# Optimization experiments

Hardware: AMD Instinct MI355X
Metric: run time of the kernel (lower is better)

The kernel has to match this reference:

```python
import jax, jax.numpy as jnp
import numpy as np

B, T, I, H = 64, 512, 256, 256


def setup_inputs() -> dict:
    key = jax.random.key(0)
    ks = jax.random.split(key, 5)
    s = 1.0 / np.sqrt(H)
    return {
        "x": jax.random.normal(ks[0], (B, T, I), dtype=jnp.float32),
        "W_ih": jax.random.uniform(ks[1], (4 * H, I), jnp.float32, -s, s),
        "W_hh": jax.random.uniform(ks[2], (4 * H, H), jnp.float32, -s, s),
        "b_ih": jax.random.uniform(ks[3], (4 * H,), jnp.float32, -s, s),
        "b_hh": jax.random.uniform(ks[4], (4 * H,), jnp.float32, -s, s),
    }


def reference(x, W_ih, W_hh, b_ih, b_hh):
    # PyTorch LSTM gate order: input, forget, cell(g), output.
    # Precompute input projection for all timesteps: [B, T, 4H]
    x_proj = jnp.einsum("bti,gi->btg", x, W_ih) + b_ih + b_hh

    def step(carry, xt):
        h, c = carry                       # [B, H] each
        gates = xt + h @ W_hh.T            # [B, 4H]
        i, f, g, o = jnp.split(gates, 4, axis=-1)
        i = jax.nn.sigmoid(i)
        f = jax.nn.sigmoid(f)
        g = jnp.tanh(g)
        o = jax.nn.sigmoid(o)
        c = f * c + i * g
        h = o * jnp.tanh(c)
        return (h, c), h

    h0 = jnp.zeros((x.shape[0], W_hh.shape[1]), x.dtype)
    c0 = jnp.zeros_like(h0)
    (hT, cT), ys = jax.lax.scan(step, (h0, c0), jnp.swapaxes(x_proj, 0, 1))
    y = jnp.swapaxes(ys, 0, 1)             # [B, T, H], batch_first
    # Matches torch: (output, (h_n, c_n)) with num_layers*num_dirs = 1
    return y, hT[None], cT[None]
```

## Files before the change

kernel.cpp:

```cpp
#include <hip/hip_runtime.h>
#include <hip/hip_bf16.h>
#include <stdint.h>

#define Bz 64
#define Tz 512
#define Iz 256
#define Hz 256
#define G4z 1024
#define YSZ (Bz*Tz*Hz)

typedef __bf16 bf16;
typedef float  f32x4  __attribute__((ext_vector_type(4)));
typedef int    i32x4  __attribute__((ext_vector_type(4)));
typedef __bf16 bf16x8 __attribute__((ext_vector_type(8)));
typedef __bf16 bf16x4 __attribute__((ext_vector_type(4)));

#define XP_OFF  0u
#define XB_OFF  67108864u
#define WI_OFF  83886080u

__global__ __launch_bounds__(256) void cvt_f32_bf16(const float* __restrict__ in,
                                                    bf16* __restrict__ out, int n4) {
  int i = blockIdx.x * blockDim.x + threadIdx.x;
  if (i >= n4) return;
  float4 v = reinterpret_cast<const float4*>(in)[i];
  bf16x4 o = {(__bf16)v.x, (__bf16)v.y, (__bf16)v.z, (__bf16)v.w};
  *reinterpret_cast<bf16x4*>(out + (size_t)i*4) = o;
}

__global__ __launch_bounds__(256) void xproj_gemm(const bf16* __restrict__ A,
                                                  const bf16* __restrict__ Bw,
                                                  const float* __restrict__ b_ih,
                                                  const float* __restrict__ b_hh,
                                                  bf16* __restrict__ xp) {
  constexpr int K = 256;
  __shared__ __align__(16) bf16 As[128*32];
  __shared__ __align__(16) bf16 Bs[128*32];
  __shared__ float bias_s[128];
  const int bm = blockIdx.x >> 3;
  const int bn = blockIdx.x & 7;
  const int m0 = bm * 128, n0 = bn * 128;
  const int tid = threadIdx.x;
  if (tid < 128) bias_s[tid] = b_ih[n0 + tid] + b_hh[n0 + tid];
  const int w = tid >> 6, lane = tid & 63;
  const int wm = w >> 1, wn = w & 1;
  const int lr = lane & 15, lk = lane >> 4;
  f32x4 acc[4][4] = {};
  for (int kt = 0; kt < 8; ++kt) {
#pragma unroll
    for (int p = 0; p < 2; ++p) {
      int elem = p * 256 + tid;
      int row = elem >> 2, c = elem & 3;
      uint4 va = *reinterpret_cast<const uint4*>(A + (size_t)(m0 + row) * K + kt*32 + c*8);
      *reinterpret_cast<uint4*>((char*)As + row*64 + ((c ^ (row & 3)) * 16)) = va;
      uint4 vb = *reinterpret_cast<const uint4*>(Bw + (size_t)(n0 + row) * K + kt*32 + c*8);
      *reinterpret_cast<uint4*>((char*)Bs + row*64 + ((c ^ (row & 3)) * 16)) = vb;
    }
    __syncthreads();
    bf16x8 fa[4], fb[4];
#pragma unroll
    for (int f = 0; f < 4; ++f) {
      int ra = wm*64 + f*16 + lr;
      fa[f] = *reinterpret_cast<const bf16x8*>((char*)As + ra*64 + ((lk ^ (ra & 3)) * 16));
      int rb = wn*64 + f*16 + lr;
      fb[f] = *reinterpret_cast<const bf16x8*>((char*)Bs + rb*64 + ((lk ^ (rb & 3)) * 16));
    }
#pragma unroll
    for (int fi = 0; fi < 4; ++fi)
#pragma unroll
      for (int fj = 0; fj < 4; ++fj)
        acc[fi][fj] = __builtin_amdgcn_mfma_f32_16x16x32_bf16(fa[fi], fb[fj], acc[fi][fj], 0, 0, 0);
    __syncthreads();
  }
#pragma unroll
  for (int fi = 0; fi < 4; ++fi)
#pragma unroll
    for (int fj = 0; fj < 4; ++fj) {
      int col = n0 + wn*64 + fj*16 + lr;
      float bias = bias_s[wn*64 + fj*16 + lr];
#pragma unroll
      for (int v = 0; v < 4; ++v) {
        int row = m0 + wm*64 + fi*16 + lk*4 + v;
        xp[(size_t)row * 1024 + col] = (__bf16)(acc[fi][fj][v] + bias);
      }
    }
}


__device__ __forceinline__ float fast_sigmoid(float x) {
  return __builtin_amdgcn_rcpf(1.f + __expf(-x));
}
__device__ __forceinline__ float fast_tanh(float x) {
  return 1.f - 2.f * __builtin_amdgcn_rcpf(__expf(2.f * x) + 1.f);
}
__device__ __forceinline__ int sdot4f(int a, int b, int c) {
#if __has_builtin(__builtin_amdgcn_sdot4)
  return __builtin_amdgcn_sdot4(a, b, c, false);
#else
  int r = c;
  r += (int)(signed char)(a)        * (int)(signed char)(b);
  r += (int)(signed char)(a >> 8)   * (int)(signed char)(b >> 8);
  r += (int)(signed char)(a >> 16)  * (int)(signed char)(b >> 16);
  r += (int)(signed char)(a >> 24)  * (int)(signed char)(b >> 24);
  return r;
#endif
}
#define SCL (1.0f / (2032.0f * 127.0f))

__global__ __launch_bounds__(512, 2) void lstm_rec(const bf16* __restrict__ xp,
                                                   const float* __restrict__ Whh,
                                                   float* __restrict__ out) {
  __shared__ __align__(16) char  h_s[256];
  __shared__ float gates[1024];
  const int tid = threadIdx.x;
  const int b = blockIdx.x;

  int w0[64], w1[64];
  {
    const float* wp0 = Whh + (size_t)tid * 256;
    const float* wp1 = Whh + (size_t)(tid + 512) * 256;
#pragma unroll
    for (int d = 0; d < 64; ++d) {
      float4 f = *reinterpret_cast<const float4*>(wp0 + d*4);
      int q0 = (int)rintf(f.x * 2032.f), q1 = (int)rintf(f.y * 2032.f);
      int q2 = (int)rintf(f.z * 2032.f), q3 = (int)rintf(f.w * 2032.f);
      w0[d] = (q0 & 255) | ((q1 & 255) << 8) | ((q2 & 255) << 16) | ((q3 & 255) << 24);
      float4 g = *reinterpret_cast<const float4*>(wp1 + d*4);
      int p0 = (int)rintf(g.x * 2032.f), p1 = (int)rintf(g.y * 2032.f);
      int p2 = (int)rintf(g.z * 2032.f), p3 = (int)rintf(g.w * 2032.f);
      w1[d] = (p0 & 255) | ((p1 & 255) << 8) | ((p2 & 255) << 16) | ((p3 & 255) << 24);
    }
  }
  if (tid < 64) reinterpret_cast<int*>(h_s)[tid] = 0;

  const bf16* xprow = xp + (size_t)b * Tz * 1024;
  unsigned short x0v = *(const unsigned short*)(xprow + tid);
  unsigned short x1v = *(const unsigned short*)(xprow + 512 + tid);

  float cc = 0.f;
  __syncthreads();

  for (int t = 0; t < Tz; ++t) {
    int a0=0,a1=0,a2=0,a3=0, d0=0,d1=0,d2=0,d3=0;
#pragma unroll
    for (int d = 0; d < 16; ++d) {
      i32x4 hv = *reinterpret_cast<const i32x4*>(h_s + d*16);
      a0 = sdot4f(hv[0], w0[4*d+0], a0);
      a1 = sdot4f(hv[1], w0[4*d+1], a1);
      a2 = sdot4f(hv[2], w0[4*d+2], a2);
      a3 = sdot4f(hv[3], w0[4*d+3], a3);
      d0 = sdot4f(hv[0], w1[4*d+0], d0);
      d1 = sdot4f(hv[1], w1[4*d+1], d1);
      d2 = sdot4f(hv[2], w1[4*d+2], d2);
      d3 = sdot4f(hv[3], w1[4*d+3], d3);
    }
    float x0f = __uint_as_float((unsigned)x0v << 16);
    float x1f = __uint_as_float((unsigned)x1v << 16);
    gates[tid]       = (float)((a0 + a1) + (a2 + a3)) * SCL + x0f;
    gates[tid + 512] = (float)((d0 + d1) + (d2 + d3)) * SCL + x1f;
    if (t < Tz - 1) {
      x0v = *(const unsigned short*)(xprow + (size_t)(t+1)*1024 + tid);
      x1v = *(const unsigned short*)(xprow + (size_t)(t+1)*1024 + 512 + tid);
    }
    __syncthreads();

    if (tid < 256) {
      float gi = fast_sigmoid(gates[tid]);
      float gf = fast_sigmoid(gates[256 + tid]);
      float gg = fast_tanh(gates[512 + tid]);
      float go = fast_sigmoid(gates[768 + tid]);
      cc = gf * cc + gi * gg;
      float hv = go * fast_tanh(cc);
      out[((size_t)b * Tz + t) * 256 + tid] = hv;
      if (t < Tz - 1) {
        h_s[tid] = (char)(int)rintf(hv * 127.f);
      } else {
        out[(size_t)YSZ + (size_t)b * 256 + tid] = hv;
        out[(size_t)YSZ + 16384 + (size_t)b * 256 + tid] = cc;
      }
    }
    __syncthreads();
  }
}

extern "C" void kernel_launch(void* const* d_in, const int* in_sizes, int n_in,
                              void* d_out, int out_size, void* d_ws, size_t ws_size,
                              hipStream_t stream) {
  const float* x    = (const float*)d_in[0];
  const float* W_ih = (const float*)d_in[1];
  const float* W_hh = (const float*)d_in[2];
  const float* b_ih = (const float*)d_in[3];
  const float* b_hh = (const float*)d_in[4];
  float* out = (float*)d_out;
  char* ws = (char*)d_ws;

  bf16* xp  = (bf16*)(ws + XP_OFF);
  bf16* xb  = (bf16*)(ws + XB_OFF);
  bf16* wib = (bf16*)(ws + WI_OFF);

  cvt_f32_bf16<<<8192, 256, 0, stream>>>(x, xb, (Bz*Tz*Iz) / 4);
  cvt_f32_bf16<<<256, 256, 0, stream>>>(W_ih, wib, (G4z*Iz) / 4);
  xproj_gemm<<<2048, 256, 0, stream>>>(xb, wib, b_ih, b_hh, xp);
  lstm_rec<<<64, 512, 0, stream>>>(xp, W_hh, out);
}
```

Before: 573.4 us.

## Exchange LSTM gates via lane shuffles and double-buffer hidden state

Thread pairs now own all four gate rows for one hidden unit (i/f in one lane, g/o in the neighbor), so the gate values are exchanged with a lane xor shuffle instead of going through a shared-memory gates array. The hidden-state buffer is double-buffered, which removes one of the two block-wide barriers per timestep. Both lanes of each pair compute the cell update redundantly, and only the even lane writes outputs. This trades some duplicated transcendental work for shorter per-step serialization.

Result: slower. 604.3 us (+5.4%).

```diff
diff --git a/kernel.cpp b/kernel.cpp
--- a/kernel.cpp
+++ b/kernel.cpp
@@ -110,15 +110,18 @@
 __global__ __launch_bounds__(512, 2) void lstm_rec(const bf16* __restrict__ xp,
                                                    const float* __restrict__ Whh,
                                                    float* __restrict__ out) {
-  __shared__ __align__(16) char  h_s[256];
-  __shared__ float gates[1024];
+  __shared__ __align__(16) char h_s[2][256];
   const int tid = threadIdx.x;
   const int b = blockIdx.x;
+  const int h = tid >> 1;
+  const int sel = tid & 1;
+  const int r0 = sel * 256 + h;
+  const int r1 = r0 + 512;
 
   int w0[64], w1[64];
   {
-    const float* wp0 = Whh + (size_t)tid * 256;
-    const float* wp1 = Whh + (size_t)(tid + 512) * 256;
+    const float* wp0 = Whh + (size_t)r0 * 256;
+    const float* wp1 = Whh + (size_t)r1 * 256;
 #pragma unroll
     for (int d = 0; d < 64; ++d) {
       float4 f = *reinterpret_cast<const float4*>(wp0 + d*4);
@@ -131,20 +134,21 @@
       w1[d] = (p0 & 255) | ((p1 & 255) << 8) | ((p2 & 255) << 16) | ((p3 & 255) << 24);
     }
   }
-  if (tid < 64) reinterpret_cast<int*>(h_s)[tid] = 0;
+  if (tid < 64) reinterpret_cast<int*>(h_s[0])[tid] = 0;
 
   const bf16* xprow = xp + (size_t)b * Tz * 1024;
-  unsigned short x0v = *(const unsigned short*)(xprow + tid);
-  unsigned short x1v = *(const unsigned short*)(xprow + 512 + tid);
+  unsigned short xv0 = *(const unsigned short*)(xprow + r0);
+  unsigned short xv1 = *(const unsigned short*)(xprow + r1);
 
   float cc = 0.f;
   __syncthreads();
 
   for (int t = 0; t < Tz; ++t) {
+    const char* hb = h_s[t & 1];
     int a0=0,a1=0,a2=0,a3=0, d0=0,d1=0,d2=0,d3=0;
 #pragma unroll
     for (int d = 0; d < 16; ++d) {
-      i32x4 hv = *reinterpret_cast<const i32x4*>(h_s + d*16);
+      i32x4 hv = *reinterpret_cast<const i32x4*>(hb + d*16);
       a0 = sdot4f(hv[0], w0[4*d+0], a0);
       a1 = sdot4f(hv[1], w0[4*d+1], a1);
       a2 = sdot4f(hv[2], w0[4*d+2], a2);
@@ -154,29 +158,31 @@
       d2 = sdot4f(hv[2], w1[4*d+2], d2);
       d3 = sdot4f(hv[3], w1[4*d+3], d3);
     }
-    float x0f = __uint_as_float((unsigned)x0v << 16);
-    float x1f = __uint_as_float((unsigned)x1v << 16);
-    gates[tid]       = (float)((a0 + a1) + (a2 + a3)) * SCL + x0f;
-    gates[tid + 512] = (float)((d0 + d1) + (d2 + d3)) * SCL + x1f;
+    float g0 = (float)((a0 + a1) + (a2 + a3)) * SCL + __uint_as_float((unsigned)xv0 << 16);
+    float g1 = (float)((d0 + d1) + (d2 + d3)) * SCL + __uint_as_float((unsigned)xv1 << 16);
     if (t < Tz - 1) {
-      x0v = *(const unsigned short*)(xprow + (size_t)(t+1)*1024 + tid);
-      x1v = *(const unsigned short*)(xprow + (size_t)(t+1)*1024 + 512 + tid);
-    }
-    __syncthreads();
-
-    if (tid < 256) {
-      float gi = fast_sigmoid(gates[tid]);
-      float gf = fast_sigmoid(gates[256 + tid]);
-      float gg = fast_tanh(gates[512 + tid]);
-      float go = fast_sigmoid(gates[768 + tid]);
-      cc = gf * cc + gi * gg;
-      float hv = go * fast_tanh(cc);
-      out[((size_t)b * Tz + t) * 256 + tid] = hv;
+      xv0 = *(const unsigned short*)(xprow + (size_t)(t+1)*1024 + r0);
+      xv1 = *(const unsigned short*)(xprow + (size_t)(t+1)*1024 + r1);
+    }
+    float p0 = __shfl_xor(g0, 1);
+    float p1 = __shfl_xor(g1, 1);
+    float vi = sel ? p0 : g0;
+    float vf = sel ? g0 : p0;
+    float vg = sel ? p1 : g1;
+    float vo = sel ? g1 : p1;
+    float gi = fast_sigmoid(vi);
+    float gf = fast_sigmoid(vf);
+    float gg = fast_tanh(vg);
+    float go = fast_sigmoid(vo);
+    cc = gf * cc + gi * gg;
+    float hv = go * fast_tanh(cc);
+    if (!sel) {
+      out[((size_t)b * Tz + t) * 256 + h] = hv;
       if (t < Tz - 1) {
-        h_s[tid] = (char)(int)rintf(hv * 127.f);
+        h_s[(t & 1) ^ 1][h] = (char)(int)rintf(hv * 127.f);
       } else {
-        out[(size_t)YSZ + (size_t)b * 256 + tid] = hv;
-        out[(size_t)YSZ + 16384 + (size_t)b * 256 + tid] = cc;
+        out[(size_t)YSZ + (size_t)b * 256 + h] = hv;
+        out[(size_t)YSZ + 16384 + (size_t)b * 256 + h] = cc;
       }
     }
     __syncthreads();
```

## Use 1024 threads per batch in recurrence with gate-interleaved layout

Applied to the files above, without the earlier changes.

The recurrent kernel now launches 1024 threads per batch row, so each thread computes one gate row instead of two. This halves the serial dot-product chain per timestep. The four gates of each hidden unit are laid out next to each other in shared memory, so the elementwise stage reads them with a single float4 load. In exchange the block now has 16 waves, which makes each barrier more expensive.

After: 580.8 us. About the same (+1.3%).

```diff
diff --git a/kernel.cpp b/kernel.cpp
--- a/kernel.cpp
+++ b/kernel.cpp
@@ -107,68 +107,58 @@
 }
 #define SCL (1.0f / (2032.0f * 127.0f))
 
-__global__ __launch_bounds__(512, 2) void lstm_rec(const bf16* __restrict__ xp,
-                                                   const float* __restrict__ Whh,
-                                                   float* __restrict__ out) {
+__global__ __launch_bounds__(1024, 1) void lstm_rec(const bf16* __restrict__ xp,
+                                                    const float* __restrict__ Whh,
+                                                    float* __restrict__ out) {
   __shared__ __align__(16) char  h_s[256];
-  __shared__ float gates[1024];
+  __shared__ __align__(16) float gates[1024];
   const int tid = threadIdx.x;
   const int b = blockIdx.x;
+  const int h = tid >> 2;
+  const int q = tid & 3;
+  const int r = q * 256 + h;
 
-  int w0[64], w1[64];
+  int w[64];
   {
-    const float* wp0 = Whh + (size_t)tid * 256;
-    const float* wp1 = Whh + (size_t)(tid + 512) * 256;
+    const float* wp = Whh + (size_t)r * 256;
 #pragma unroll
     for (int d = 0; d < 64; ++d) {
-      float4 f = *reinterpret_cast<const float4*>(wp0 + d*4);
+      float4 f = *reinterpret_cast<const float4*>(wp + d*4);
       int q0 = (int)rintf(f.x * 2032.f), q1 = (int)rintf(f.y * 2032.f);
       int q2 = (int)rintf(f.z * 2032.f), q3 = (int)rintf(f.w * 2032.f);
-      w0[d] = (q0 & 255) | ((q1 & 255) << 8) | ((q2 & 255) << 16) | ((q3 & 255) << 24);
-      float4 g = *reinterpret_cast<const float4*>(wp1 + d*4);
-      int p0 = (int)rintf(g.x * 2032.f), p1 = (int)rintf(g.y * 2032.f);
-      int p2 = (int)rintf(g.z * 2032.f), p3 = (int)rintf(g.w * 2032.f);
-      w1[d] = (p0 & 255) | ((p1 & 255) << 8) | ((p2 & 255) << 16) | ((p3 & 255) << 24);
+      w[d] = (q0 & 255) | ((q1 & 255) << 8) | ((q2 & 255) << 16) | ((q3 & 255) << 24);
     }
   }
   if (tid < 64) reinterpret_cast<int*>(h_s)[tid] = 0;
 
   const bf16* xprow = xp + (size_t)b * Tz * 1024;
-  unsigned short x0v = *(const unsigned short*)(xprow + tid);
-  unsigned short x1v = *(const unsigned short*)(xprow + 512 + tid);
+  unsigned short xv = *(const unsigned short*)(xprow + r);
 
   float cc = 0.f;
   __syncthreads();
 
   for (int t = 0; t < Tz; ++t) {
-    int a0=0,a1=0,a2=0,a3=0, d0=0,d1=0,d2=0,d3=0;
+    int a0 = 0, a1 = 0, a2 = 0, a3 = 0;
 #pragma unroll
     for (int d = 0; d < 16; ++d) {
       i32x4 hv = *reinterpret_cast<const i32x4*>(h_s + d*16);
-      a0 = sdot4f(hv[0], w0[4*d+0], a0);
-      a1 = sdot4f(hv[1], w0[4*d+1], a1);
-      a2 = sdot4f(hv[2], w0[4*d+2], a2);
-      a3 = sdot4f(hv[3], w0[4*d+3], a3);
-      d0 = sdot4f(hv[0], w1[4*d+0], d0);
-      d1 = sdot4f(hv[1], w1[4*d+1], d1);
-      d2 = sdot4f(hv[2], w1[4*d+2], d2);
-      d3 = sdot4f(hv[3], w1[4*d+3], d3);
+      a0 = sdot4f(hv[0], w[4*d+0], a0);
+      a1 = sdot4f(hv[1], w[4*d+1], a1);
+      a2 = sdot4f(hv[2], w[4*d+2], a2);
+      a3 = sdot4f(hv[3], w[4*d+3], a3);
     }
-    float x0f = __uint_as_float((unsigned)x0v << 16);
-    float x1f = __uint_as_float((unsigned)x1v << 16);
-    gates[tid]       = (float)((a0 + a1) + (a2 + a3)) * SCL + x0f;
-    gates[tid + 512] = (float)((d0 + d1) + (d2 + d3)) * SCL + x1f;
-    if (t < Tz - 1) {
-      x0v = *(const unsigned short*)(xprow + (size_t)(t+1)*1024 + tid);
-      x1v = *(const unsigned short*)(xprow + (size_t)(t+1)*1024 + 512 + tid);
-    }
+    float xcur = __uint_as_float((unsigned)xv << 16);
+    if (t < Tz - 1)
+      xv = *(const unsigned short*)(xprow + (size_t)(t+1)*1024 + r);
+    gates[tid] = (float)((a0 + a1) + (a2 + a3)) * SCL + xcur;
     __syncthreads();
 
     if (tid < 256) {
-      float gi = fast_sigmoid(gates[tid]);
-      float gf = fast_sigmoid(gates[256 + tid]);
-      float gg = fast_tanh(gates[512 + tid]);
-      float go = fast_sigmoid(gates[768 + tid]);
+      float4 g4 = *reinterpret_cast<const float4*>(gates + tid*4);
+      float gi = fast_sigmoid(g4.x);
+      float gf = fast_sigmoid(g4.y);
+      float gg = fast_tanh(g4.z);
+      float go = fast_sigmoid(g4.w);
       cc = gf * cc + gi * gg;
       float hv = go * fast_tanh(cc);
       out[((size_t)b * Tz + t) * 256 + tid] = hv;
@@ -201,5 +191,5 @@
   cvt_f32_bf16<<<8192, 256, 0, stream>>>(x, xb, (Bz*Tz*Iz) / 4);
   cvt_f32_bf16<<<256, 256, 0, stream>>>(W_ih, wib, (G4z*Iz) / 4);
   xproj_gemm<<<2048, 256, 0, stream>>>(xb, wib, b_ih, b_hh, xp);
-  lstm_rec<<<64, 512, 0, stream>>>(xp, W_hh, out);
+  lstm_rec<<<64, 1024, 0, stream>>>(xp, W_hh, out);
 }
```
